# Performance work log

Measured on AMD Instinct MI355X. Metric: run time of the kernel, lower is better.

Reference implementation:

```python
import jax, jax.numpy as jnp
import numpy as np
from math import sqrt

B, S, E, H = 4, 2048, 1024, 16
D = E // H  # per-head dim = 64


def setup_inputs() -> dict:
    key = jax.random.key(0)
    ks = jax.random.split(key, 11)
    f = lambda k, shape, scale=1.0: jax.random.normal(k, shape, dtype=jnp.float32) * scale
    return {
        "Q": f(ks[0], (B, S, E)),
        "K": f(ks[1], (B, S, E)),
        "V": f(ks[2], (B, S, E)),
        "Wq": f(ks[3], (E, E), 1.0 / sqrt(E)),
        "bq": f(ks[4], (E,), 0.02),
        "Wk": f(ks[5], (E, E), 1.0 / sqrt(E)),
        "bk": f(ks[6], (E,), 0.02),
        "Wv": f(ks[7], (E, E), 1.0 / sqrt(E)),
        "bv": f(ks[8], (E,), 0.02),
        "Wo": f(ks[9], (E, E), 1.0 / sqrt(E)),
        "bo": f(ks[10], (E,), 0.02),
    }


def reference(Q, K, V, Wq, bq, Wk, bk, Wv, bv, Wo, bo):
    # Linear projections (torch Linear: x @ W.T + b)
    q = Q @ Wq.T + bq  # [B,S,E]
    k = K @ Wk.T + bk
    v = V @ Wv.T + bv
    # torch.chunk along last dim into H heads == reshape [B,S,H,D]
    q = q.reshape(B, S, H, D)
    k = k.reshape(B, S, H, D)
    v = v.reshape(B, S, H, D)
    scale = 1.0 / sqrt(D)
    # batched-over-heads scaled dot-product attention
    scores = jnp.einsum("bqhd,bkhd->bhqk", q, k) * scale  # [B,H,S,S]
    attn = jax.nn.softmax(scores, axis=-1)
    out = jnp.einsum("bhqk,bkhd->bqhd", attn, v).reshape(B, S, E)
    # dropout p=0.0 -> identity
    return out @ Wo.T + bo
```

## Files before the change

kernel.cpp:

```cpp
#include <hip/hip_runtime.h>
#include <hip/hip_bf16.h>

#define B_SZ   4
#define S_LEN  2048
#define E_DIM  1024
#define H_NUM  16
#define D_DIM  64
#define M_ROWS (B_SZ * S_LEN)
#define QK_SCALE 0.1803368801111204f

typedef __attribute__((ext_vector_type(8))) __bf16 bf16x8;
typedef __attribute__((ext_vector_type(4))) float  f32x4;

__device__ __forceinline__ bf16x8 load8(const void* p) {
    return __builtin_bit_cast(bf16x8, *reinterpret_cast<const uint4*>(p));
}

#if defined(__has_builtin)
#if __has_builtin(__builtin_amdgcn_exp2f)
#define EXP2F(x) __builtin_amdgcn_exp2f(x)
#endif
#if __has_builtin(__builtin_amdgcn_global_load_lds)
#define HAVE_GLL 1
#endif
#endif
#ifndef EXP2F
#define EXP2F(x) exp2f(x)
#endif

__device__ __forceinline__ void stage16(const __hip_bfloat16* g, __hip_bfloat16* lbase, int lane) {
#ifdef HAVE_GLL
    __builtin_amdgcn_global_load_lds((const __attribute__((address_space(1))) unsigned int*)g,
                                     (__attribute__((address_space(3))) unsigned int*)lbase,
                                     16, 0, 0);
#else
    reinterpret_cast<uint4*>(lbase)[lane] = *reinterpret_cast<const uint4*>(g);
#endif
}

#define N8A (1 << 20)
#define N8W (1 << 17)
#define N8TOT (3 * N8A + 4 * N8W)

struct CvtArgs {
    const float* s[7];
    __hip_bfloat16* d[7];
};

__global__ __launch_bounds__(256) void cvt_all(CvtArgs a)
{
    const int i = blockIdx.x * 256 + threadIdx.x;
    if (i >= N8TOT) return;
    int seg, off;
    if (i < 3 * N8A) { seg = i >> 20;              off = i & (N8A - 1); }
    else             { const int j = i - 3 * N8A;
                       seg = 3 + (j >> 17);        off = j & (N8W - 1); }
    const float* s = a.s[seg];
    __hip_bfloat16* d = a.d[seg];
    const float4 x = reinterpret_cast<const float4*>(s)[off * 2];
    const float4 y = reinterpret_cast<const float4*>(s)[off * 2 + 1];
    __hip_bfloat16 o[8];
    o[0] = __float2bfloat16(x.x); o[1] = __float2bfloat16(x.y);
    o[2] = __float2bfloat16(x.z); o[3] = __float2bfloat16(x.w);
    o[4] = __float2bfloat16(y.x); o[5] = __float2bfloat16(y.y);
    o[6] = __float2bfloat16(y.z); o[7] = __float2bfloat16(y.w);
    reinterpret_cast<uint4*>(d)[off] = *reinterpret_cast<uint4*>(o);
}

__global__ __launch_bounds__(256) void cvt_f32_bf16(const float* __restrict__ s,
                                                    __hip_bfloat16* __restrict__ d,
                                                    int n8)
{
    const int i = blockIdx.x * 256 + threadIdx.x;
    if (i >= n8) return;
    const float4 a = reinterpret_cast<const float4*>(s)[i * 2];
    const float4 b = reinterpret_cast<const float4*>(s)[i * 2 + 1];
    __hip_bfloat16 o[8];
    o[0] = __float2bfloat16(a.x); o[1] = __float2bfloat16(a.y);
    o[2] = __float2bfloat16(a.z); o[3] = __float2bfloat16(a.w);
    o[4] = __float2bfloat16(b.x); o[5] = __float2bfloat16(b.y);
    o[6] = __float2bfloat16(b.z); o[7] = __float2bfloat16(b.w);
    reinterpret_cast<uint4*>(d)[i] = *reinterpret_cast<uint4*>(o);
}

struct GemmArgs {
    const __hip_bfloat16* A[3];
    const __hip_bfloat16* W[3];
    const float* bias[3];
    void* C[3];
    float scale[3];
    int mode[3];
};

__global__ __launch_bounds__(512, 4) void gemm_bt(GemmArgs g)
{
    __shared__ __attribute__((aligned(16))) char lds_raw[3 * 24576];

    const int tid = threadIdx.x;
    const int wid = tid >> 6, lane = tid & 63;
    const int quad = lane >> 4, l16 = lane & 15;
    const int wm = wid >> 2, wn = wid & 3;

    const int seg = blockIdx.x >> 8;
    int bid = blockIdx.x & 255;
    bid = (bid & 7) * 32 + (bid >> 3);
    const int bm = bid >> 2, bn = bid & 3;
    const int row0 = bm * 128, col0 = bn * 256;

    const __hip_bfloat16* A = g.A[seg];
    const __hip_bfloat16* W = g.W[seg];

    const int s_line = tid >> 3, s_gr = tid & 7;
    const int glin  = s_gr ^ (s_line & 7);
    const int s_row = (s_line << 1) + (glin >> 2);
    const int s_ks  = glin & 3;
    const __hip_bfloat16* gA = A + (size_t)(row0 + s_row) * E_DIM + s_ks * 8;
    const __hip_bfloat16* gB = W + (size_t)(col0 + s_row) * E_DIM + s_ks * 8;
    const int stA = wid << 10;

    const int rg   = (((l16 & 1) << 2) | quad) ^ ((l16 >> 1) & 7);
    const int aoff = (wm * 32 + (l16 >> 1)) * 128 + rg * 16;
    const int boff = (wn * 32 + (l16 >> 1)) * 128 + rg * 16;

    f32x4 acc[4][4];
    const f32x4 zero = {0.f, 0.f, 0.f, 0.f};
#pragma unroll
    for (int i = 0; i < 4; i++)
#pragma unroll
        for (int j = 0; j < 4; j++) acc[i][j] = zero;

    auto stage_t = [&](int t) {
        char* b = lds_raw + (t % 3) * 24576;
        const int ko = t * 32;
        stage16(gA + ko, (__hip_bfloat16*)(b + stA), lane);
        stage16(gB + ko, (__hip_bfloat16*)(b + 8192 + stA), lane);
        stage16(gB + (size_t)128 * E_DIM + ko, (__hip_bfloat16*)(b + 16384 + stA), lane);
    };

    auto body = [&](int t, bool stg) {
        __builtin_amdgcn_s_barrier();
        __builtin_amdgcn_sched_barrier(0);
        if (stg) stage_t(t + 2);
        const char* ab = lds_raw + (t % 3) * 24576;
        bf16x8 af[4], bf[4];
#pragma unroll
        for (int i = 0; i < 4; i++) af[i] = load8(ab + aoff + i * 1024);
#pragma unroll
        for (int j = 0; j < 4; j++) bf[j] = load8(ab + 8192 + boff + j * 1024);
        __builtin_amdgcn_s_setprio(1);
#pragma unroll
        for (int i = 0; i < 4; i++)
#pragma unroll
            for (int j = 0; j < 4; j++)
                acc[i][j] = __builtin_amdgcn_mfma_f32_16x16x32_bf16(af[i], bf[j], acc[i][j], 0, 0, 0);
        __builtin_amdgcn_s_setprio(0);
        __builtin_amdgcn_sched_barrier(0);
    };

    const int NT = E_DIM / 32;
    stage_t(0); stage_t(1);
    for (int t = 0; t < NT - 2; ++t) {
        asm volatile("s_waitcnt vmcnt(3)" ::: "memory");
        body(t, true);
    }
    asm volatile("s_waitcnt vmcnt(3)" ::: "memory"); body(NT - 2, false);
    asm volatile("s_waitcnt vmcnt(0)" ::: "memory"); body(NT - 1, false);

    const int   mode  = g.mode[seg];
    const float scale = g.scale[seg];
    const float* bias = g.bias[seg];
    void* Cout        = g.C[seg];
#pragma unroll
    for (int j = 0; j < 4; j++) {
        const int col = col0 + wn * 64 + j * 16 + l16;
        const float bv = bias[col];
#pragma unroll
        for (int i = 0; i < 4; i++) {
            const int row = row0 + wm * 64 + i * 16 + quad * 4;
            if (mode == 3) {
                __attribute__((aligned(8))) __hip_bfloat16 o[4];
#pragma unroll
                for (int r = 0; r < 4; r++) o[r] = __float2bfloat16((acc[i][j][r] + bv) * scale);
                const int b_ = row >> 11, s_ = row & 2047, h_ = col >> 6, d_ = col & 63;
                *reinterpret_cast<uint2*>((__hip_bfloat16*)Cout +
                    (((size_t)(b_ * H_NUM + h_)) << 17) + (d_ << 11) + s_) =
                    *reinterpret_cast<uint2*>(o);
            } else {
#pragma unroll
                for (int r = 0; r < 4; r++) {
                    const float v = (acc[i][j][r] + bv) * scale;
                    const int rr = row + r;
                    if (mode == 0) {
                        ((__hip_bfloat16*)Cout)[(size_t)rr * E_DIM + col] = __float2bfloat16(v);
                    } else if (mode == 1) {
                        ((float*)Cout)[(size_t)rr * E_DIM + col] = v;
                    } else {
                        const int b_ = rr >> 11, s_ = rr & 2047, h_ = col >> 6, d_ = col & 63;
                        ((__hip_bfloat16*)Cout)[(((size_t)(b_ * H_NUM + h_)) << 17) + (s_ << 6) + d_] =
                            __float2bfloat16(v);
                    }
                }
            }
        }
    }
}

__global__ __launch_bounds__(256) void attn(const __hip_bfloat16* __restrict__ Qt,
                                            const __hip_bfloat16* __restrict__ Kt,
                                            const __hip_bfloat16* __restrict__ Vt,
                                            __hip_bfloat16* __restrict__ Op)
{
    __shared__ __hip_bfloat16 Pls[4][64][40];

    const int x = blockIdx.x;
    const int xcd = x & 7, idx = x >> 3;
    const int bh     = xcd * 8 + (idx & 7);
    const int qchunk = idx >> 3;
    const int wave = threadIdx.x >> 6, lane = threadIdx.x & 63;
    const int quad = lane >> 4, l16 = lane & 15;
    const int qrow0 = qchunk * 256 + wave * 64;

    const __hip_bfloat16* qb = Qt + ((size_t)bh << 17);
    const __hip_bfloat16* kb = Kt + ((size_t)bh << 17);
    const __hip_bfloat16* vb = Vt + ((size_t)bh << 17);
    __hip_bfloat16* pw = &Pls[wave][0][0];

    bf16x8 qf[4][2];
#pragma unroll
    for (int qt = 0; qt < 4; qt++) {
        qf[qt][0] = load8(qb + ((qrow0 + qt * 16 + l16) << 6) + quad * 8);
        qf[qt][1] = load8(qb + ((qrow0 + qt * 16 + l16) << 6) + 32 + quad * 8);
    }

    const f32x4 zero = {0.f, 0.f, 0.f, 0.f};
    f32x4 o_acc[4][4];
#pragma unroll
    for (int qt = 0; qt < 4; qt++)
#pragma unroll
        for (int dj = 0; dj < 4; dj++) o_acc[qt][dj] = zero;
    float lsum[4] = {0.f, 0.f, 0.f, 0.f};

    bf16x8 kaA[2], kcA[2], vfA[4], kaB[2], kcB[2], vfB[4];

    auto prefetch = [&](bf16x8 (&ka)[2], bf16x8 (&kc)[2], bf16x8 (&vf)[4], int kv) {
#pragma unroll
        for (int t = 0; t < 2; t++) {
            ka[t] = load8(kb + ((kv + t * 16 + l16) << 6) + quad * 8);
            kc[t] = load8(kb + ((kv + t * 16 + l16) << 6) + 32 + quad * 8);
        }
#pragma unroll
        for (int dj = 0; dj < 4; dj++)
            vf[dj] = load8(vb + ((size_t)(dj * 16 + l16) << 11) + kv + quad * 8);
    };

    auto compute = [&](const bf16x8 (&ka)[2], const bf16x8 (&kc)[2], const bf16x8 (&vf)[4]) {
#pragma unroll
        for (int t = 0; t < 2; t++) {
#pragma unroll
            for (int qt = 0; qt < 4; qt++) {
                f32x4 st = __builtin_amdgcn_mfma_f32_16x16x32_bf16(ka[t], qf[qt][0], zero, 0, 0, 0);
                st       = __builtin_amdgcn_mfma_f32_16x16x32_bf16(kc[t], qf[qt][1], st, 0, 0, 0);
                const float p0 = EXP2F(st[0]), p1 = EXP2F(st[1]);
                const float p2 = EXP2F(st[2]), p3 = EXP2F(st[3]);
                lsum[qt] += (p0 + p1) + (p2 + p3);
                const unsigned u0 = (unsigned)__bfloat16_as_ushort(__float2bfloat16(p0));
                const unsigned u1 = (unsigned)__bfloat16_as_ushort(__float2bfloat16(p1));
                const unsigned u2 = (unsigned)__bfloat16_as_ushort(__float2bfloat16(p2));
                const unsigned u3 = (unsigned)__bfloat16_as_ushort(__float2bfloat16(p3));
                uint2 w;
                w.x = (u1 << 16) | u0;
                w.y = (u3 << 16) | u2;
                *reinterpret_cast<uint2*>(&pw[(qt * 16 + l16) * 40 + t * 16 + quad * 4]) = w;
            }
        }
        __builtin_amdgcn_s_setprio(1);
#pragma unroll
        for (int qt = 0; qt < 4; qt++) {
            const bf16x8 pa = load8(&pw[(qt * 16 + l16) * 40 + quad * 8]);
#pragma unroll
            for (int dj = 0; dj < 4; dj++)
                o_acc[qt][dj] = __builtin_amdgcn_mfma_f32_16x16x32_bf16(pa, vf[dj], o_acc[qt][dj], 0, 0, 0);
        }
        __builtin_amdgcn_s_setprio(0);
    };

    prefetch(kaA, kcA, vfA, 0);
    for (int kv0 = 0; kv0 < S_LEN; kv0 += 64) {
        prefetch(kaB, kcB, vfB, (kv0 + 32) & (S_LEN - 1));
        __builtin_amdgcn_sched_barrier(0);
        compute(kaA, kcA, vfA);
        prefetch(kaA, kcA, vfA, (kv0 + 64) & (S_LEN - 1));
        __builtin_amdgcn_sched_barrier(0);
        compute(kaB, kcB, vfB);
    }

    const int b_ = bh >> 4, h_ = bh & 15;
#pragma unroll
    for (int qt = 0; qt < 4; qt++) {
        float l = lsum[qt];
        l += __shfl_xor(l, 16, 64);
        l += __shfl_xor(l, 32, 64);
#pragma unroll
        for (int r = 0; r < 4; r++) {
            const float lr = __shfl(l, quad * 4 + r, 64);
            const float inv = 1.f / lr;
            const size_t ro = ((size_t)b_ * S_LEN + (qrow0 + qt * 16 + quad * 4 + r)) * E_DIM + h_ * D_DIM;
#pragma unroll
            for (int dj = 0; dj < 4; dj++)
                Op[ro + dj * 16 + l16] = __float2bfloat16(o_acc[qt][dj][r] * inv);
        }
    }
}

extern "C" void kernel_launch(void* const* d_in, const int* in_sizes, int n_in,
                              void* d_out, int out_size, void* d_ws, size_t ws_size,
                              hipStream_t stream)
{
    const float* Qf  = (const float*)d_in[0];
    const float* Kf  = (const float*)d_in[1];
    const float* Vf  = (const float*)d_in[2];
    const float* Wqf = (const float*)d_in[3];
    const float* bqf = (const float*)d_in[4];
    const float* Wkf = (const float*)d_in[5];
    const float* bkf = (const float*)d_in[6];
    const float* Wvf = (const float*)d_in[7];
    const float* bvf = (const float*)d_in[8];
    const float* Wof = (const float*)d_in[9];
    const float* bof = (const float*)d_in[10];

    const size_t n_act = (size_t)M_ROWS * E_DIM;
    const size_t n_w   = (size_t)E_DIM * E_DIM;

    const dim3 blk(256), gblk(512), ablk(256);
    const int cg_act = (int)(n_act / 8 / 256);
    const int cg_w   = (int)(n_w / 8 / 256);

    const size_t need_fast = (6 * n_act + 4 * n_w) * sizeof(__hip_bfloat16);

    if (ws_size >= need_fast) {
        __hip_bfloat16* Xq = (__hip_bfloat16*)d_ws;
        __hip_bfloat16* Xk = Xq + n_act;
        __hip_bfloat16* Xv = Xk + n_act;
        __hip_bfloat16* Wb = Xv + n_act;
        __hip_bfloat16* Qt = Wb + 4 * n_w;
        __hip_bfloat16* Kt = Qt + n_act;
        __hip_bfloat16* Vt = Kt + n_act;

        CvtArgs ca;
        ca.s[0] = Qf;  ca.s[1] = Kf;  ca.s[2] = Vf;
        ca.s[3] = Wqf; ca.s[4] = Wkf; ca.s[5] = Wvf; ca.s[6] = Wof;
        ca.d[0] = Xq;  ca.d[1] = Xk;  ca.d[2] = Xv;
        ca.d[3] = Wb;  ca.d[4] = Wb + n_w; ca.d[5] = Wb + 2 * n_w; ca.d[6] = Wb + 3 * n_w;
        cvt_all<<<dim3(N8TOT / 256), blk, 0, stream>>>(ca);

        GemmArgs qkv;
        qkv.A[0] = Xq;  qkv.A[1] = Xk;  qkv.A[2] = Xv;
        qkv.W[0] = Wb;  qkv.W[1] = Wb + n_w;  qkv.W[2] = Wb + 2*n_w;
        qkv.bias[0] = bqf;  qkv.bias[1] = bkf;  qkv.bias[2] = bvf;
        qkv.C[0] = Qt;  qkv.C[1] = Kt;  qkv.C[2] = Vt;
        qkv.scale[0] = QK_SCALE;  qkv.scale[1] = 1.0f;  qkv.scale[2] = 1.0f;
        qkv.mode[0] = 2;  qkv.mode[1] = 2;  qkv.mode[2] = 3;
        gemm_bt<<<dim3(768), gblk, 0, stream>>>(qkv);

        attn<<<dim3(512), ablk, 0, stream>>>(Qt, Kt, Vt, Xq);

        GemmArgs og;
        og.A[0] = Xq;  og.A[1] = Xq;  og.A[2] = Xq;
        og.W[0] = Wb + 3*n_w;  og.W[1] = og.W[0];  og.W[2] = og.W[0];
        og.bias[0] = bof;  og.bias[1] = bof;  og.bias[2] = bof;
        og.C[0] = d_out;  og.C[1] = d_out;  og.C[2] = d_out;
        og.scale[0] = 1.0f;  og.scale[1] = 1.0f;  og.scale[2] = 1.0f;
        og.mode[0] = 1;  og.mode[1] = 1;  og.mode[2] = 1;
        gemm_bt<<<dim3(256), gblk, 0, stream>>>(og);
    } else {
        __hip_bfloat16* X  = (__hip_bfloat16*)d_ws;
        __hip_bfloat16* Wb = X + n_act;
        __hip_bfloat16* Qt = Wb + n_w;
        __hip_bfloat16* Kt = Qt + n_act;
        __hip_bfloat16* Vt = Kt + n_act;

        auto one = [&](const float* Af, const float* Wf, const float* bf_,
                       void* C, float sc, int md) {
            cvt_f32_bf16<<<cg_act, blk, 0, stream>>>(Af, X, (int)(n_act / 8));
            cvt_f32_bf16<<<cg_w,   blk, 0, stream>>>(Wf, Wb, (int)(n_w / 8));
            GemmArgs a;
            a.A[0] = X; a.A[1] = X; a.A[2] = X;
            a.W[0] = Wb; a.W[1] = Wb; a.W[2] = Wb;
            a.bias[0] = bf_; a.bias[1] = bf_; a.bias[2] = bf_;
            a.C[0] = C; a.C[1] = C; a.C[2] = C;
            a.scale[0] = sc; a.scale[1] = sc; a.scale[2] = sc;
            a.mode[0] = md; a.mode[1] = md; a.mode[2] = md;
            gemm_bt<<<dim3(256), gblk, 0, stream>>>(a);
        };
        one(Qf, Wqf, bqf, Qt, QK_SCALE, 2);
        one(Kf, Wkf, bkf, Kt, 1.0f, 2);
        one(Vf, Wvf, bvf, Vt, 1.0f, 3);
        attn<<<dim3(512), ablk, 0, stream>>>(Qt, Kt, Vt, X);
        cvt_f32_bf16<<<cg_w, blk, 0, stream>>>(Wof, Wb, (int)(n_w / 8));
        GemmArgs og;
        og.A[0] = X; og.A[1] = X; og.A[2] = X;
        og.W[0] = Wb; og.W[1] = Wb; og.W[2] = Wb;
        og.bias[0] = bof; og.bias[1] = bof; og.bias[2] = bof;
        og.C[0] = d_out; og.C[1] = d_out; og.C[2] = d_out;
        og.scale[0] = 1.0f; og.scale[1] = 1.0f; og.scale[2] = 1.0f;
        og.mode[0] = 1; og.mode[1] = 1; og.mode[2] = 1;
        gemm_bt<<<dim3(256), gblk, 0, stream>>>(og);
    }
}
```

Before: 367.0 us.

## Shrink GEMM tile to 128x128 with 256-thread blocks and double buffering

The projection GEMM kernel goes from 512-thread blocks with 128x256 tiles and a three-stage LDS ring to 256-thread blocks with 128x128 tiles and a plain two-buffer pipeline synchronised by __syncthreads. The XOR-swizzled LDS layout, the manual vmcnt waits and the setprio hints are removed, and the grid sizes double to match. The aim is more blocks and simpler scheduling. In exchange, each loaded tile is reused less, LDS bank conflicts are likely without the swizzle, and a full barrier every k-step leaves less overlap between loads and MFMA work.

New measurement: 388.6 us. 1.06x slower.

```diff
diff --git a/kernel.cpp b/kernel.cpp
--- a/kernel.cpp
+++ b/kernel.cpp
@@ -92,35 +92,28 @@
     int mode[3];
 };
 
-__global__ __launch_bounds__(512, 4) void gemm_bt(GemmArgs g)
-{
-    __shared__ __attribute__((aligned(16))) char lds_raw[3 * 24576];
+__global__ __launch_bounds__(256) void gemm_bt(GemmArgs g)
+{
+    __shared__ __attribute__((aligned(16))) __hip_bfloat16 lds[2][2][128 * 32];
 
     const int tid = threadIdx.x;
     const int wid = tid >> 6, lane = tid & 63;
     const int quad = lane >> 4, l16 = lane & 15;
-    const int wm = wid >> 2, wn = wid & 3;
-
-    const int seg = blockIdx.x >> 8;
-    int bid = blockIdx.x & 255;
-    bid = (bid & 7) * 32 + (bid >> 3);
-    const int bm = bid >> 2, bn = bid & 3;
-    const int row0 = bm * 128, col0 = bn * 256;
+    const int wm = wid >> 1, wn = wid & 1;
+
+    const int seg = blockIdx.x >> 9;
+    int bid = blockIdx.x & 511;
+    bid = (bid & 7) * 64 + (bid >> 3);
+    const int bm = bid >> 3, bn = bid & 7;
+    const int row0 = bm * 128, col0 = bn * 128;
 
     const __hip_bfloat16* A = g.A[seg];
     const __hip_bfloat16* W = g.W[seg];
 
-    const int s_line = tid >> 3, s_gr = tid & 7;
-    const int glin  = s_gr ^ (s_line & 7);
-    const int s_row = (s_line << 1) + (glin >> 2);
-    const int s_ks  = glin & 3;
-    const __hip_bfloat16* gA = A + (size_t)(row0 + s_row) * E_DIM + s_ks * 8;
-    const __hip_bfloat16* gB = W + (size_t)(col0 + s_row) * E_DIM + s_ks * 8;
-    const int stA = wid << 10;
-
-    const int rg   = (((l16 & 1) << 2) | quad) ^ ((l16 >> 1) & 7);
-    const int aoff = (wm * 32 + (l16 >> 1)) * 128 + rg * 16;
-    const int boff = (wn * 32 + (l16 >> 1)) * 128 + rg * 16;
+    const int rS = tid >> 2, ksS = (tid & 3) * 8;
+    const __hip_bfloat16* gAp = A + (size_t)(row0 + rS) * E_DIM + ksS;
+    const __hip_bfloat16* gBp = W + (size_t)(col0 + rS) * E_DIM + ksS;
+    const int stW = wid << 10;
 
     f32x4 acc[4][4];
     const f32x4 zero = {0.f, 0.f, 0.f, 0.f};
@@ -129,42 +122,36 @@
 #pragma unroll
         for (int j = 0; j < 4; j++) acc[i][j] = zero;
 
-    auto stage_t = [&](int t) {
-        char* b = lds_raw + (t % 3) * 24576;
+    auto stage = [&](int t, int buf) {
         const int ko = t * 32;
-        stage16(gA + ko, (__hip_bfloat16*)(b + stA), lane);
-        stage16(gB + ko, (__hip_bfloat16*)(b + 8192 + stA), lane);
-        stage16(gB + (size_t)128 * E_DIM + ko, (__hip_bfloat16*)(b + 16384 + stA), lane);
+        char* bA = (char*)&lds[buf][0][0];
+        char* bB = (char*)&lds[buf][1][0];
+        stage16(gAp + ko,                      (__hip_bfloat16*)(bA + stW), lane);
+        stage16(gAp + (size_t)64 * E_DIM + ko, (__hip_bfloat16*)(bA + 4096 + stW), lane);
+        stage16(gBp + ko,                      (__hip_bfloat16*)(bB + stW), lane);
+        stage16(gBp + (size_t)64 * E_DIM + ko, (__hip_bfloat16*)(bB + 4096 + stW), lane);
     };
 
-    auto body = [&](int t, bool stg) {
-        __builtin_amdgcn_s_barrier();
-        __builtin_amdgcn_sched_barrier(0);
-        if (stg) stage_t(t + 2);
-        const char* ab = lds_raw + (t % 3) * 24576;
+    const int NT = E_DIM / 32;
+    stage(0, 0);
+    int cur = 0;
+    for (int t = 0; t < NT; ++t) {
+        __syncthreads();
+        if (t + 1 < NT) stage(t + 1, cur ^ 1);
+        const char* bA = (const char*)&lds[cur][0][0];
+        const char* bB = (const char*)&lds[cur][1][0];
         bf16x8 af[4], bf[4];
 #pragma unroll
-        for (int i = 0; i < 4; i++) af[i] = load8(ab + aoff + i * 1024);
-#pragma unroll
-        for (int j = 0; j < 4; j++) bf[j] = load8(ab + 8192 + boff + j * 1024);
-        __builtin_amdgcn_s_setprio(1);
+        for (int i = 0; i < 4; i++) af[i] = load8(bA + (wm * 64 + i * 16 + l16) * 64 + quad * 16);
+#pragma unroll
+        for (int j = 0; j < 4; j++) bf[j] = load8(bB + (wn * 64 + j * 16 + l16) * 64 + quad * 16);
 #pragma unroll
         for (int i = 0; i < 4; i++)
 #pragma unroll
             for (int j = 0; j < 4; j++)
                 acc[i][j] = __builtin_amdgcn_mfma_f32_16x16x32_bf16(af[i], bf[j], acc[i][j], 0, 0, 0);
-        __builtin_amdgcn_s_setprio(0);
-        __builtin_amdgcn_sched_barrier(0);
-    };
-
-    const int NT = E_DIM / 32;
-    stage_t(0); stage_t(1);
-    for (int t = 0; t < NT - 2; ++t) {
-        asm volatile("s_waitcnt vmcnt(3)" ::: "memory");
-        body(t, true);
-    }
-    asm volatile("s_waitcnt vmcnt(3)" ::: "memory"); body(NT - 2, false);
-    asm volatile("s_waitcnt vmcnt(0)" ::: "memory"); body(NT - 1, false);
+        cur ^= 1;
+    }
 
     const int   mode  = g.mode[seg];
     const float scale = g.scale[seg];
@@ -331,7 +318,7 @@
     const size_t n_act = (size_t)M_ROWS * E_DIM;
     const size_t n_w   = (size_t)E_DIM * E_DIM;
 
-    const dim3 blk(256), gblk(512), ablk(256);
+    const dim3 blk(256), ablk(256);
     const int cg_act = (int)(n_act / 8 / 256);
     const int cg_w   = (int)(n_w / 8 / 256);
 
@@ -360,7 +347,7 @@
         qkv.C[0] = Qt;  qkv.C[1] = Kt;  qkv.C[2] = Vt;
         qkv.scale[0] = QK_SCALE;  qkv.scale[1] = 1.0f;  qkv.scale[2] = 1.0f;
         qkv.mode[0] = 2;  qkv.mode[1] = 2;  qkv.mode[2] = 3;
-        gemm_bt<<<dim3(768), gblk, 0, stream>>>(qkv);
+        gemm_bt<<<dim3(1536), blk, 0, stream>>>(qkv);
 
         attn<<<dim3(512), ablk, 0, stream>>>(Qt, Kt, Vt, Xq);
 
@@ -371,7 +358,7 @@
         og.C[0] = d_out;  og.C[1] = d_out;  og.C[2] = d_out;
         og.scale[0] = 1.0f;  og.scale[1] = 1.0f;  og.scale[2] = 1.0f;
         og.mode[0] = 1;  og.mode[1] = 1;  og.mode[2] = 1;
-        gemm_bt<<<dim3(256), gblk, 0, stream>>>(og);
+        gemm_bt<<<dim3(512), blk, 0, stream>>>(og);
     } else {
         __hip_bfloat16* X  = (__hip_bfloat16*)d_ws;
         __hip_bfloat16* Wb = X + n_act;
@@ -390,7 +377,7 @@
             a.C[0] = C; a.C[1] = C; a.C[2] = C;
             a.scale[0] = sc; a.scale[1] = sc; a.scale[2] = sc;
             a.mode[0] = md; a.mode[1] = md; a.mode[2] = md;
-            gemm_bt<<<dim3(256), gblk, 0, stream>>>(a);
+            gemm_bt<<<dim3(512), blk, 0, stream>>>(a);
         };
         one(Qf, Wqf, bqf, Qt, QK_SCALE, 2);
         one(Kf, Wkf, bkf, Kt, 1.0f, 2);
@@ -404,6 +391,6 @@
         og.C[0] = d_out; og.C[1] = d_out; og.C[2] = d_out;
         og.scale[0] = 1.0f; og.scale[1] = 1.0f; og.scale[2] = 1.0f;
         og.mode[0] = 1; og.mode[1] = 1; og.mode[2] = 1;
-        gemm_bt<<<dim3(256), gblk, 0, stream>>>(og);
-    }
-}
+        gemm_bt<<<dim3(512), blk, 0, stream>>>(og);
+    }
+}
```

## Stage K/V tiles through swizzled shared memory shared by all waves

Applied to the files above, without the earlier changes.

The attention kernel now cooperatively loads each 32-key K and V tile into double-buffered, XOR-swizzled LDS (using the existing stage16 helper) instead of having every wave load K/V fragments directly from global memory into registers. This removes the fourfold redundant global/L2 traffic across the four waves of a block and frees registers previously used for double-buffered fragments. In exchange, a block-wide __syncthreads is added every 32 keys and reads now go through LDS, which may serialize waves and reduce latency hiding.

After: 331.4 us. -9.7%, faster.

```diff
diff --git a/kernel.cpp b/kernel.cpp
--- a/kernel.cpp
+++ b/kernel.cpp
@@ -211,12 +211,15 @@
                                             __hip_bfloat16* __restrict__ Op)
 {
     __shared__ __hip_bfloat16 Pls[4][64][40];
+    __shared__ __attribute__((aligned(16))) __hip_bfloat16 Kls[2][32 * 64];
+    __shared__ __attribute__((aligned(16))) __hip_bfloat16 Vls[2][64 * 32];
 
     const int x = blockIdx.x;
     const int xcd = x & 7, idx = x >> 3;
     const int bh     = xcd * 8 + (idx & 7);
     const int qchunk = idx >> 3;
-    const int wave = threadIdx.x >> 6, lane = threadIdx.x & 63;
+    const int tid = threadIdx.x;
+    const int wave = tid >> 6, lane = tid & 63;
     const int quad = lane >> 4, l16 = lane & 15;
     const int qrow0 = qchunk * 256 + wave * 64;
 
@@ -225,6 +228,14 @@
     const __hip_bfloat16* vb = Vt + ((size_t)bh << 17);
     __hip_bfloat16* pw = &Pls[wave][0][0];
 
+    const int skey = tid >> 3, sgk = (tid & 7) ^ (skey & 7);
+    const __hip_bfloat16* kSrc = kb + (skey << 6) + (sgk << 3);
+    const int sd = tid >> 2, sgv = (tid & 3) ^ ((sd >> 1) & 3);
+    const __hip_bfloat16* vSrc = vb + ((size_t)sd << 11) + (sgv << 3);
+    const int stW = wave << 10;
+
+    const int ksw = l16 & 7, vsw = (l16 >> 1) & 3;
+
     bf16x8 qf[4][2];
 #pragma unroll
     for (int qt = 0; qt < 4; qt++) {
@@ -240,26 +251,22 @@
         for (int dj = 0; dj < 4; dj++) o_acc[qt][dj] = zero;
     float lsum[4] = {0.f, 0.f, 0.f, 0.f};
 
-    bf16x8 kaA[2], kcA[2], vfA[4], kaB[2], kcB[2], vfB[4];
-
-    auto prefetch = [&](bf16x8 (&ka)[2], bf16x8 (&kc)[2], bf16x8 (&vf)[4], int kv) {
+    auto stageKV = [&](int kv, int b) {
+        stage16(kSrc + (kv << 6), (__hip_bfloat16*)((char*)&Kls[b][0] + stW), lane);
+        stage16(vSrc + kv,        (__hip_bfloat16*)((char*)&Vls[b][0] + stW), lane);
+    };
+
+    auto compute = [&](int b) {
+        const char* Kbuf = (const char*)&Kls[b][0];
+        const char* Vbuf = (const char*)&Vls[b][0];
 #pragma unroll
         for (int t = 0; t < 2; t++) {
-            ka[t] = load8(kb + ((kv + t * 16 + l16) << 6) + quad * 8);
-            kc[t] = load8(kb + ((kv + t * 16 + l16) << 6) + 32 + quad * 8);
-        }
-#pragma unroll
-        for (int dj = 0; dj < 4; dj++)
-            vf[dj] = load8(vb + ((size_t)(dj * 16 + l16) << 11) + kv + quad * 8);
-    };
-
-    auto compute = [&](const bf16x8 (&ka)[2], const bf16x8 (&kc)[2], const bf16x8 (&vf)[4]) {
-#pragma unroll
-        for (int t = 0; t < 2; t++) {
+            const bf16x8 ka = load8(Kbuf + ((t * 16 + l16) << 7) + ((quad ^ ksw) << 4));
+            const bf16x8 kc = load8(Kbuf + ((t * 16 + l16) << 7) + (((quad + 4) ^ ksw) << 4));
 #pragma unroll
             for (int qt = 0; qt < 4; qt++) {
-                f32x4 st = __builtin_amdgcn_mfma_f32_16x16x32_bf16(ka[t], qf[qt][0], zero, 0, 0, 0);
-                st       = __builtin_amdgcn_mfma_f32_16x16x32_bf16(kc[t], qf[qt][1], st, 0, 0, 0);
+                f32x4 st = __builtin_amdgcn_mfma_f32_16x16x32_bf16(ka, qf[qt][0], zero, 0, 0, 0);
+                st       = __builtin_amdgcn_mfma_f32_16x16x32_bf16(kc, qf[qt][1], st, 0, 0, 0);
                 const float p0 = EXP2F(st[0]), p1 = EXP2F(st[1]);
                 const float p2 = EXP2F(st[2]), p3 = EXP2F(st[3]);
                 lsum[qt] += (p0 + p1) + (p2 + p3);
@@ -273,6 +280,10 @@
                 *reinterpret_cast<uint2*>(&pw[(qt * 16 + l16) * 40 + t * 16 + quad * 4]) = w;
             }
         }
+        bf16x8 vf[4];
+#pragma unroll
+        for (int dj = 0; dj < 4; dj++)
+            vf[dj] = load8(Vbuf + ((dj * 16 + l16) << 6) + ((quad ^ vsw) << 4));
         __builtin_amdgcn_s_setprio(1);
 #pragma unroll
         for (int qt = 0; qt < 4; qt++) {
@@ -284,14 +295,13 @@
         __builtin_amdgcn_s_setprio(0);
     };
 
-    prefetch(kaA, kcA, vfA, 0);
-    for (int kv0 = 0; kv0 < S_LEN; kv0 += 64) {
-        prefetch(kaB, kcB, vfB, (kv0 + 32) & (S_LEN - 1));
-        __builtin_amdgcn_sched_barrier(0);
-        compute(kaA, kcA, vfA);
-        prefetch(kaA, kcA, vfA, (kv0 + 64) & (S_LEN - 1));
-        __builtin_amdgcn_sched_barrier(0);
-        compute(kaB, kcB, vfB);
+    stageKV(0, 0);
+    int cur = 0;
+    for (int kv0 = 0; kv0 < S_LEN; kv0 += 32) {
+        __syncthreads();
+        if (kv0 + 32 < S_LEN) stageKV(kv0 + 32, cur ^ 1);
+        compute(cur);
+        cur ^= 1;
     }
 
     const int b_ = bh >> 4, h_ = bh & 15;
```
